# Optimization experiments

Hardware: AMD Instinct MI355X
Metric: run time of the kernel (lower is better)

## Reference

```python
import jax, jax.numpy as jnp
import numpy as np

N_NODES = 50000
N_EDGES = 800000


def gcn_layer(x, edge_index, W, b):
    """PyG-style GCNConv: add self-loops, symmetric deg^-1/2 normalization,
    linear transform, scatter-sum aggregation at target nodes, plus bias."""
    n = x.shape[0]
    loops = jnp.arange(n)
    src = jnp.concatenate([edge_index[0], loops])  # [E+N]
    dst = jnp.concatenate([edge_index[1], loops])  # [E+N]
    deg = jax.ops.segment_sum(jnp.ones(src.shape, dtype=x.dtype), dst, num_segments=n)
    dinv = jnp.where(deg > 0, jax.lax.rsqrt(deg), jnp.zeros((), x.dtype))
    norm = dinv[src] * dinv[dst]               # [E+N]
    h = x @ W                                   # [N, out]
    msg = norm[:, None] * h[src]                # [E+N, out] gather
    out = jax.ops.segment_sum(msg, dst, num_segments=n)  # scatter-add
    return out + b


def setup_inputs() -> dict:
    key = jax.random.key(0)
    ks = jax.random.split(key, 8)
    features = jax.random.normal(ks[0], (N_NODES, 64), dtype=jnp.float32)
    edge_index1 = jax.random.randint(ks[1], (2, N_EDGES), 0, N_NODES)
    edge_index3 = jax.random.randint(ks[2], (2, N_EDGES), 0, N_NODES)
    edge_index9 = jax.random.randint(ks[3], (2, N_EDGES), 0, N_NODES)

    def glorot(k, fi, fo):
        lim = float(np.sqrt(6.0 / (fi + fo)))
        return jax.random.uniform(k, (fi, fo), minval=-lim, maxval=lim, dtype=jnp.float32)

    W1 = glorot(ks[4], 64, 64)
    W2 = glorot(ks[5], 64, 32)
    W3 = glorot(ks[6], 32, 16)
    b1 = jnp.zeros((64,), jnp.float32)
    b2 = jnp.zeros((32,), jnp.float32)
    b3 = jnp.zeros((16,), jnp.float32)
    return dict(features=features, edge_index1=edge_index1, edge_index3=edge_index3,
                edge_index9=edge_index9, W1=W1, b1=b1, W2=W2, b2=b2, W3=W3, b3=b3)


def reference(features, edge_index1, edge_index3, edge_index9, W1, b1, W2, b2, W3, b3):
    x = jax.nn.relu(gcn_layer(features, edge_index1, W1, b1))  # hop 1
    x = jax.nn.relu(gcn_layer(x, edge_index3, W2, b2))         # hop 3
    x = jax.nn.relu(gcn_layer(x, edge_index9, W3, b3))         # hop 9
    return x
```

## Files before the change

kernel.cpp:

```cpp
#include <hip/hip_runtime.h>
#include <hip/hip_fp16.h>


#define NB   256
#define NL   3
#define TB   (NB * NL)
#define CAPE 6400
#define CAPE_E (CAPE + 8)
#define CH   8192
#define P1T  512
#define EPT  (CH / P1T)
#define P2T  512

__device__ __forceinline__ void decode_chunk(int g, int nc1, int nc2,
                                             const int* s1, const int* d1, int E1,
                                             const int* s2, const int* d2, int E2,
                                             const int* s3, const int* d3, int E3,
                                             const int** src, const int** dst, int* E, int* l,
                                             int* gout) {
    if (g < nc1)            { *src = s1; *dst = d1; *E = E1; *l = 0; }
    else if (g < nc1 + nc2) { *src = s2; *dst = d2; *E = E2; *l = 1; g -= nc1; }
    else                    { *src = s3; *dst = d3; *E = E3; *l = 2; g -= nc1 + nc2; }
    *gout = g;
}

__device__ __forceinline__ void fma4(float4& a, float s, const float4& w) {
    a.x += s * w.x; a.y += s * w.y; a.z += s * w.z; a.w += s * w.w;
}
__device__ __forceinline__ void add4(float4& a, const float4& v) {
    a.x += v.x; a.y += v.y; a.z += v.z; a.w += v.w;
}
__device__ __forceinline__ float4 ldh4(const __half* h, size_t idx4) {
    uint2 r = ((const uint2*)h)[idx4];
    __half2 a = *reinterpret_cast<__half2*>(&r.x);
    __half2 b = *reinterpret_cast<__half2*>(&r.y);
    float2 fa = __half22float2(a), fb = __half22float2(b);
    return make_float4(fa.x, fa.y, fb.x, fb.y);
}
__device__ __forceinline__ void sth4(__half* h, size_t idx4, float4 v) {
    __half2 a = __floats2half2_rn(v.x, v.y);
    __half2 b = __floats2half2_rn(v.z, v.w);
    uint2 r;
    r.x = *reinterpret_cast<unsigned*>(&a);
    r.y = *reinterpret_cast<unsigned*>(&b);
    ((uint2*)h)[idx4] = r;
}

__global__ void __launch_bounds__(P1T) phase1(
        const int* __restrict__ s1, const int* __restrict__ d1, int E1,
        const int* __restrict__ s2, const int* __restrict__ d2, int E2,
        const int* __restrict__ s3, const int* __restrict__ d3, int E3,
        int nc1, int nc2, int W,
        int* __restrict__ gcur, unsigned int* __restrict__ pairBuf) {
    __shared__ int hist[TB];
    __shared__ int bo[TB];
    __shared__ int lcur[TB];
    for (int i = threadIdx.x; i < TB; i += P1T) hist[i] = 0;
    __syncthreads();
    const int* src; const int* dst; int E, l, g;
    decode_chunk(blockIdx.x, nc1, nc2, s1, d1, E1, s2, d2, E2, s3, d3, E3,
                 &src, &dst, &E, &l, &g);
    const int e0 = g * CH;
    const int lbase = l * NB;
    unsigned pv[EPT];
    int bn[EPT];
    if (E - e0 >= CH) {
        const int4* s4 = (const int4*)(src + e0);
        const int4* d4 = (const int4*)(dst + e0);
#pragma unroll
        for (int w = 0; w < EPT / 4; ++w) {
            int4 sv = s4[threadIdx.x + w * P1T];
            int4 dv = d4[threadIdx.x + w * P1T];
            int q, i = w * 4;
            q = dv.x / W; bn[i+0] = lbase + q; pv[i+0] = ((unsigned)sv.x << 9) | (unsigned)(dv.x - q * W);
            q = dv.y / W; bn[i+1] = lbase + q; pv[i+1] = ((unsigned)sv.y << 9) | (unsigned)(dv.y - q * W);
            q = dv.z / W; bn[i+2] = lbase + q; pv[i+2] = ((unsigned)sv.z << 9) | (unsigned)(dv.z - q * W);
            q = dv.w / W; bn[i+3] = lbase + q; pv[i+3] = ((unsigned)sv.w << 9) | (unsigned)(dv.w - q * W);
        }
    } else {
#pragma unroll
        for (int i = 0; i < EPT; ++i) {
            int e = e0 + threadIdx.x + i * P1T;
            if (e < E) {
                int s = src[e], d = dst[e];
                int q = d / W;
                bn[i] = lbase + q;
                pv[i] = ((unsigned)s << 9) | (unsigned)(d - q * W);
            } else bn[i] = -1;
        }
    }
#pragma unroll
    for (int i = 0; i < EPT; ++i)
        if (bn[i] >= 0) atomicAdd(&hist[bn[i]], 1);
    __syncthreads();
    for (int i = threadIdx.x; i < TB; i += P1T) {
        int c = hist[i];
        bo[i] = i * CAPE + (c ? atomicAdd(&gcur[i], c) : 0);
        lcur[i] = 0;
    }
    __syncthreads();
#pragma unroll
    for (int i = 0; i < EPT; ++i) {
        if (bn[i] >= 0) {
            int r = atomicAdd(&lcur[bn[i]], 1);
            int pos = bo[bn[i]] + r;
            if (pos < (bn[i] + 1) * CAPE) pairBuf[pos] = pv[i];
        }
    }
}

__global__ void __launch_bounds__(P2T) k2_phase2_gemm1(
        const unsigned int* __restrict__ pairBuf, const int* __restrict__ gcur,
        int n, int W,
        int* __restrict__ row_ptr, int* __restrict__ cnt_g,
        float* __restrict__ dinv, unsigned short* __restrict__ eidx,
        const float* __restrict__ x0, const float* __restrict__ W1g,
        __half* __restrict__ h1) {
    __shared__ __align__(16) char smem[17408];
    if (blockIdx.x < (unsigned)TB) {
        int* lcnt  = (int*)smem;
        int* lscan = lcnt + P2T;
        unsigned short* stage = (unsigned short*)(lscan + P2T);
        const int bid = blockIdx.x;
        const int l = bid / NB, k = bid % NB;
        const int lo = k * W;
        const int hi = min(n, lo + W);
        const int Wn = hi - lo;
        const int segE = min(gcur[bid], CAPE);
        const size_t base  = (size_t)bid * CAPE;
        const int    baseE = bid * CAPE_E;
        const int t = threadIdx.x;
        lcnt[t] = 0;
        __syncthreads();
        for (int i = t; i < segE; i += P2T)
            atomicAdd(&lcnt[pairBuf[base + i] & 511u], 1);
        __syncthreads();
        const int v = lcnt[t];
        const int vp = (v + 3) & ~3;
        lscan[t] = vp;
        __syncthreads();
        for (int off = 1; off < P2T; off <<= 1) {
            int add = (t >= off) ? lscan[t - off] : 0;
            __syncthreads();
            lscan[t] += add;
            __syncthreads();
        }
        const int pexcl = lscan[t] - vp;
        const int segEp = lscan[P2T - 1];
        if (t < Wn) {
            int node = l * n + lo + t;
            row_ptr[node] = baseE + pexcl;
            cnt_g[node] = v;
            dinv[node] = rsqrtf((float)v + 1.0f);
        }
        __syncthreads();
        lcnt[t] = pexcl;
        __syncthreads();
        const bool lds_ok = (segEp <= CAPE);
        for (int i = t; i < segE; i += P2T) {
            unsigned p = pairBuf[base + i];
            int pos = atomicAdd(&lcnt[p & 511u], 1);
            unsigned short s = (unsigned short)(p >> 9);
            if (lds_ok) stage[pos] = s;
            else if (pos < CAPE_E) eidx[baseE + pos] = s;
        }
        __syncthreads();
        if (lds_ok) {
            const int4* st4 = (const int4*)stage;
            int4* e4 = (int4*)(eidx + baseE);
            int m16 = (segEp + 7) >> 3;
            for (int i = t; i < m16; i += P2T) e4[i] = st4[i];
        }
    } else {
        float* Ws = (float*)smem;
        const int bid = blockIdx.x - TB;
        for (int i = threadIdx.x; i < 1024; i += P2T)
            ((float4*)Ws)[i] = ((const float4*)W1g)[i];
        __syncthreads();
        const int tc = threadIdx.x % 16;
        const int tr = threadIdx.x / 16;
        const int row0 = bid * 128 + tr * 4;
        const float4* x4 = (const float4*)x0;
        const float4* Ws4 = (const float4*)Ws;
        float4 acc[4];
#pragma unroll
        for (int r = 0; r < 4; ++r) acc[r] = make_float4(0.f, 0.f, 0.f, 0.f);
        int rowc[4];
#pragma unroll
        for (int r = 0; r < 4; ++r) rowc[r] = min(row0 + r, n - 1);
        for (int k0 = 0; k0 < 64; k0 += 4) {
            float4 wv0 = Ws4[(k0 + 0) * 16 + tc];
            float4 wv1 = Ws4[(k0 + 1) * 16 + tc];
            float4 wv2 = Ws4[(k0 + 2) * 16 + tc];
            float4 wv3 = Ws4[(k0 + 3) * 16 + tc];
#pragma unroll
            for (int r = 0; r < 4; ++r) {
                float4 xv = x4[(size_t)rowc[r] * 16 + (k0 / 4)];
                fma4(acc[r], xv.x, wv0);
                fma4(acc[r], xv.y, wv1);
                fma4(acc[r], xv.z, wv2);
                fma4(acc[r], xv.w, wv3);
            }
        }
#pragma unroll
        for (int r = 0; r < 4; ++r) {
            int row = row0 + r;
            if (row < n) sth4(h1, (size_t)row * 16 + tc, acc[r]);
        }
    }
}

__global__ void __launch_bounds__(256) k3_gather1_gemm2(
        const int* __restrict__ row_ptr, const int* __restrict__ cnt,
        const unsigned short* __restrict__ eidx, const float* __restrict__ dinv1,
        const float* __restrict__ dinv2,
        const __half* __restrict__ h1, const float* __restrict__ b1,
        const float* __restrict__ W2g, __half* __restrict__ h2, int n) {
    __shared__ float xs[16 * 68];
    __shared__ float W2s[64 * 32];
    for (int i = threadIdx.x; i < 512; i += 256)
        ((float4*)W2s)[i] = ((const float4*)W2g)[i];
    const int ln = threadIdx.x >> 4;
    const int f4 = threadIdx.x & 15;
    const int node = blockIdx.x * 16 + ln;
    if (node < n) {
        const int beg = row_ptr[node];
        const int m = cnt[node];
        float4 a0 = make_float4(0.f, 0.f, 0.f, 0.f), a1 = a0, a2 = a0, a3 = a0;
        int j = 0;
        for (; j + 8 <= m; j += 8) {
            ushort4 e0 = *(const ushort4*)(eidx + beg + j);
            ushort4 e1 = *(const ushort4*)(eidx + beg + j + 4);
            float w0 = dinv1[e0.x], w1 = dinv1[e0.y], w2 = dinv1[e0.z], w3 = dinv1[e0.w];
            float w4 = dinv1[e1.x], w5 = dinv1[e1.y], w6 = dinv1[e1.z], w7 = dinv1[e1.w];
            float4 v0 = ldh4(h1, (size_t)e0.x * 16 + f4);
            float4 v1 = ldh4(h1, (size_t)e0.y * 16 + f4);
            float4 v2 = ldh4(h1, (size_t)e0.z * 16 + f4);
            float4 v3 = ldh4(h1, (size_t)e0.w * 16 + f4);
            float4 v4 = ldh4(h1, (size_t)e1.x * 16 + f4);
            float4 v5 = ldh4(h1, (size_t)e1.y * 16 + f4);
            float4 v6 = ldh4(h1, (size_t)e1.z * 16 + f4);
            float4 v7 = ldh4(h1, (size_t)e1.w * 16 + f4);
            fma4(a0, w0, v0); fma4(a1, w1, v1); fma4(a2, w2, v2); fma4(a3, w3, v3);
            fma4(a0, w4, v4); fma4(a1, w5, v5); fma4(a2, w6, v6); fma4(a3, w7, v7);
        }
        if (j + 4 <= m) {
            ushort4 e0 = *(const ushort4*)(eidx + beg + j);
            fma4(a0, dinv1[e0.x], ldh4(h1, (size_t)e0.x * 16 + f4));
            fma4(a1, dinv1[e0.y], ldh4(h1, (size_t)e0.y * 16 + f4));
            fma4(a2, dinv1[e0.z], ldh4(h1, (size_t)e0.z * 16 + f4));
            fma4(a3, dinv1[e0.w], ldh4(h1, (size_t)e0.w * 16 + f4));
            j += 4;
        }
        for (; j < m; ++j) {
            int s = eidx[beg + j];
            fma4(a0, dinv1[s], ldh4(h1, (size_t)s * 16 + f4));
        }
        add4(a0, a1); add4(a2, a3); add4(a0, a2);
        float di = dinv1[node];
        float4 self = ldh4(h1, (size_t)node * 16 + f4);
        float4 bv = ((const float4*)b1)[f4];
        float4 o;
        o.x = di * (a0.x + di * self.x) + bv.x;
        o.y = di * (a0.y + di * self.y) + bv.y;
        o.z = di * (a0.z + di * self.z) + bv.z;
        o.w = di * (a0.w + di * self.w) + bv.w;
        o.x = o.x > 0.f ? o.x : 0.f;
        o.y = o.y > 0.f ? o.y : 0.f;
        o.z = o.z > 0.f ? o.z : 0.f;
        o.w = o.w > 0.f ? o.w : 0.f;
        *(float4*)&xs[ln * 68 + f4 * 4] = o;
    }
    __syncthreads();
    if (node < n) {
        const int c0 = f4 * 2;
        float s0 = 0.f, s1 = 0.f;
#pragma unroll
        for (int k = 0; k < 64; ++k) {
            float xv = xs[ln * 68 + k];
            s0 += xv * W2s[k * 32 + c0];
            s1 += xv * W2s[k * 32 + c0 + 1];
        }
        float d2 = dinv2[node];
        ((__half2*)h2)[(size_t)node * 16 + f4] = __floats2half2_rn(s0 * d2, s1 * d2);
    }
}

__global__ void __launch_bounds__(256) k4_gather2_gemm3(
        const int* __restrict__ row_ptr2, const int* __restrict__ cnt2,
        const unsigned short* __restrict__ eidx, const float* __restrict__ dinv2,
        const float* __restrict__ dinv3,
        const __half* __restrict__ h2, const float* __restrict__ b2,
        const float* __restrict__ W3g, __half* __restrict__ h3, int n) {
    __shared__ float xs[32 * 36];
    __shared__ float W3s[32 * 16];
    for (int i = threadIdx.x; i < 128; i += 256)
        ((float4*)W3s)[i] = ((const float4*)W3g)[i];
    const int ln = threadIdx.x >> 3;
    const int f4 = threadIdx.x & 7;
    const int node = blockIdx.x * 32 + ln;
    if (node < n) {
        const int beg = row_ptr2[node];
        const int m = cnt2[node];
        float4 a0 = make_float4(0.f, 0.f, 0.f, 0.f), a1 = a0, a2 = a0, a3 = a0;
        int j = 0;
        for (; j + 8 <= m; j += 8) {
            ushort4 e0 = *(const ushort4*)(eidx + beg + j);
            ushort4 e1 = *(const ushort4*)(eidx + beg + j + 4);
            add4(a0, ldh4(h2, (size_t)e0.x * 8 + f4));
            add4(a1, ldh4(h2, (size_t)e0.y * 8 + f4));
            add4(a2, ldh4(h2, (size_t)e0.z * 8 + f4));
            add4(a3, ldh4(h2, (size_t)e0.w * 8 + f4));
            add4(a0, ldh4(h2, (size_t)e1.x * 8 + f4));
            add4(a1, ldh4(h2, (size_t)e1.y * 8 + f4));
            add4(a2, ldh4(h2, (size_t)e1.z * 8 + f4));
            add4(a3, ldh4(h2, (size_t)e1.w * 8 + f4));
        }
        if (j + 4 <= m) {
            ushort4 e0 = *(const ushort4*)(eidx + beg + j);
            add4(a0, ldh4(h2, (size_t)e0.x * 8 + f4));
            add4(a1, ldh4(h2, (size_t)e0.y * 8 + f4));
            add4(a2, ldh4(h2, (size_t)e0.z * 8 + f4));
            add4(a3, ldh4(h2, (size_t)e0.w * 8 + f4));
            j += 4;
        }
        for (; j < m; ++j)
            add4(a0, ldh4(h2, (size_t)eidx[beg + j] * 8 + f4));
        add4(a0, a1); add4(a2, a3); add4(a0, a2);
        float di = dinv2[node];
        float4 self = ldh4(h2, (size_t)node * 8 + f4);
        float4 bv = ((const float4*)b2)[f4];
        float4 o;
        o.x = di * (a0.x + self.x) + bv.x;
        o.y = di * (a0.y + self.y) + bv.y;
        o.z = di * (a0.z + self.z) + bv.z;
        o.w = di * (a0.w + self.w) + bv.w;
        o.x = o.x > 0.f ? o.x : 0.f;
        o.y = o.y > 0.f ? o.y : 0.f;
        o.z = o.z > 0.f ? o.z : 0.f;
        o.w = o.w > 0.f ? o.w : 0.f;
        *(float4*)&xs[ln * 36 + f4 * 4] = o;
    }
    __syncthreads();
    if (node < n) {
        const int c0 = f4 * 2;
        float s0 = 0.f, s1 = 0.f;
#pragma unroll
        for (int k = 0; k < 32; ++k) {
            float xv = xs[ln * 36 + k];
            s0 += xv * W3s[k * 16 + c0];
            s1 += xv * W3s[k * 16 + c0 + 1];
        }
        float d3 = dinv3[node];
        ((__half2*)h3)[(size_t)node * 8 + f4] = __floats2half2_rn(s0 * d3, s1 * d3);
    }
}

__global__ void __launch_bounds__(256) k5_gather3(
        const int* __restrict__ row_ptr3, const int* __restrict__ cnt3,
        const unsigned short* __restrict__ eidx, const float* __restrict__ dinv3,
        const __half* __restrict__ h3, const float* __restrict__ b3,
        float* __restrict__ out, int n) {
    const int ln = threadIdx.x >> 2;
    const int f4 = threadIdx.x & 3;
    const int node = blockIdx.x * 64 + ln;
    if (node >= n) return;
    const int beg = row_ptr3[node];
    const int m = cnt3[node];
    float4 a0 = make_float4(0.f, 0.f, 0.f, 0.f), a1 = a0, a2 = a0, a3 = a0;
    int j = 0;
    for (; j + 8 <= m; j += 8) {
        ushort4 e0 = *(const ushort4*)(eidx + beg + j);
        ushort4 e1 = *(const ushort4*)(eidx + beg + j + 4);
        add4(a0, ldh4(h3, (size_t)e0.x * 4 + f4));
        add4(a1, ldh4(h3, (size_t)e0.y * 4 + f4));
        add4(a2, ldh4(h3, (size_t)e0.z * 4 + f4));
        add4(a3, ldh4(h3, (size_t)e0.w * 4 + f4));
        add4(a0, ldh4(h3, (size_t)e1.x * 4 + f4));
        add4(a1, ldh4(h3, (size_t)e1.y * 4 + f4));
        add4(a2, ldh4(h3, (size_t)e1.z * 4 + f4));
        add4(a3, ldh4(h3, (size_t)e1.w * 4 + f4));
    }
    if (j + 4 <= m) {
        ushort4 e0 = *(const ushort4*)(eidx + beg + j);
        add4(a0, ldh4(h3, (size_t)e0.x * 4 + f4));
        add4(a1, ldh4(h3, (size_t)e0.y * 4 + f4));
        add4(a2, ldh4(h3, (size_t)e0.z * 4 + f4));
        add4(a3, ldh4(h3, (size_t)e0.w * 4 + f4));
        j += 4;
    }
    for (; j < m; ++j)
        add4(a0, ldh4(h3, (size_t)eidx[beg + j] * 4 + f4));
    add4(a0, a1); add4(a2, a3); add4(a0, a2);
    float di = dinv3[node];
    float4 self = ldh4(h3, (size_t)node * 4 + f4);
    float4 bv = ((const float4*)b3)[f4];
    float4 o;
    o.x = di * (a0.x + self.x) + bv.x;
    o.y = di * (a0.y + self.y) + bv.y;
    o.z = di * (a0.z + self.z) + bv.z;
    o.w = di * (a0.w + self.w) + bv.w;
    o.x = o.x > 0.f ? o.x : 0.f;
    o.y = o.y > 0.f ? o.y : 0.f;
    o.z = o.z > 0.f ? o.z : 0.f;
    o.w = o.w > 0.f ? o.w : 0.f;
    ((float4*)out)[(size_t)node * 4 + f4] = o;
}

extern "C" void kernel_launch(void* const* d_in, const int* in_sizes, int n_in,
                              void* d_out, int out_size, void* d_ws, size_t ws_size,
                              hipStream_t stream) {
    const float* x0  = (const float*)d_in[0];
    const int*   ei1 = (const int*)d_in[1];
    const int*   ei3 = (const int*)d_in[2];
    const int*   ei9 = (const int*)d_in[3];
    const float* W1  = (const float*)d_in[4];
    const float* b1  = (const float*)d_in[5];
    const float* W2  = (const float*)d_in[6];
    const float* b2  = (const float*)d_in[7];
    const float* W3  = (const float*)d_in[8];
    const float* b3  = (const float*)d_in[9];

    const int n  = in_sizes[0] / 64;
    const int E1 = in_sizes[1] / 2;
    const int E3 = in_sizes[2] / 2;
    const int E9 = in_sizes[3] / 2;
    const int n3 = 3 * n;
    const int W  = (n + NB - 1) / NB;

    const int nc1 = (E1 + CH - 1) / CH;
    const int nc2 = (E3 + CH - 1) / CH;
    const int nc3 = (E9 + CH - 1) / CH;
    const int nchunks = nc1 + nc2 + nc3;
    const int gemmBlks = (n + 127) / 128;

    int* gcur    = (int*)d_ws;
    unsigned int* pairBuf = (unsigned int*)(gcur + TB);
    unsigned short* eidx = (unsigned short*)(pairBuf + (size_t)TB * CAPE);
    int* row_ptr = (int*)(eidx + (size_t)TB * CAPE_E);
    int* cnt     = row_ptr + n3;
    float* dinv  = (float*)(cnt + n3);
    __half* h1   = (__half*)(dinv + n3);
    __half* h2   = h1 + (size_t)n * 64;
    __half* h3   = h2 + (size_t)n * 32;

    hipMemsetAsync(gcur, 0, TB * sizeof(int), stream);
    phase1<<<nchunks, P1T, 0, stream>>>(ei1, ei1 + E1, E1, ei3, ei3 + E3, E3,
                                        ei9, ei9 + E9, E9, nc1, nc2, W, gcur, pairBuf);
    k2_phase2_gemm1<<<TB + gemmBlks, P2T, 0, stream>>>(
        pairBuf, gcur, n, W, row_ptr, cnt, dinv, eidx, x0, W1, h1);
    k3_gather1_gemm2<<<(n + 15) / 16, 256, 0, stream>>>(
        row_ptr, cnt, eidx, dinv, dinv + n, h1, b1, W2, h2, n);
    k4_gather2_gemm3<<<(n + 31) / 32, 256, 0, stream>>>(
        row_ptr + n, cnt + n, eidx, dinv + n, dinv + 2 * n, h2, b2, W3, h3, n);
    k5_gather3<<<(n + 63) / 64, 256, 0, stream>>>(
        row_ptr + 2 * n, cnt + 2 * n, eidx, dinv + 2 * n, h3, b3, (float*)d_out, n);
}
```

Measured before the change: 176.8 us.

## Sort nodes by degree within buckets to balance gather workloads

The phase-2 kernel now counting-sorts each bucket's nodes by descending in-degree and writes a per-layer node permutation. The three gather kernels process nodes in permuted order, so nodes of similar degree share a block and wavefront. This aims to cut divergence and tail imbalance inside warps, at the cost of an extra sort, an extra indirection load, and scattered output writes. The node ids are stored as unsigned short, so the permutation only holds while n fits in 16 bits.

```diff
diff --git a/kernel.cpp b/kernel.cpp
--- a/kernel.cpp
+++ b/kernel.cpp
@@ -114,6 +114,7 @@
         int n, int W,
         int* __restrict__ row_ptr, int* __restrict__ cnt_g,
         float* __restrict__ dinv, unsigned short* __restrict__ eidx,
+        unsigned short* __restrict__ nodeperm,
         const float* __restrict__ x0, const float* __restrict__ W1g,
         __half* __restrict__ h1) {
     __shared__ __align__(16) char smem[17408];
@@ -171,6 +172,31 @@
             int m16 = (segEp + 7) >> 3;
             for (int i = t; i < m16; i += P2T) e4[i] = st4[i];
         }
+        __syncthreads();
+        int* dcnt = lcnt;
+        int* dscan = lscan;
+        if (t < 256) dcnt[t] = 0;
+        __syncthreads();
+        int r = 0;
+        if (t < Wn) {
+            r = 255 - min(v, 255);
+            atomicAdd(&dcnt[r], 1);
+        }
+        __syncthreads();
+        if (t < 256) dscan[t] = dcnt[t];
+        __syncthreads();
+        for (int off = 1; off < 256; off <<= 1) {
+            int add = (t < 256 && t >= off) ? dscan[t - off] : 0;
+            __syncthreads();
+            if (t < 256) dscan[t] += add;
+            __syncthreads();
+        }
+        if (t < 256) dcnt[t] = dscan[t] - dcnt[t];
+        __syncthreads();
+        if (t < Wn) {
+            int slot = atomicAdd(&dcnt[r], 1);
+            nodeperm[(size_t)l * n + lo + slot] = (unsigned short)(lo + t);
+        }
     } else {
         float* Ws = (float*)smem;
         const int bid = blockIdx.x - TB;
@@ -184,28 +210,28 @@
         const float4* Ws4 = (const float4*)Ws;
         float4 acc[4];
 #pragma unroll
-        for (int r = 0; r < 4; ++r) acc[r] = make_float4(0.f, 0.f, 0.f, 0.f);
+        for (int r2 = 0; r2 < 4; ++r2) acc[r2] = make_float4(0.f, 0.f, 0.f, 0.f);
         int rowc[4];
 #pragma unroll
-        for (int r = 0; r < 4; ++r) rowc[r] = min(row0 + r, n - 1);
+        for (int r2 = 0; r2 < 4; ++r2) rowc[r2] = min(row0 + r2, n - 1);
         for (int k0 = 0; k0 < 64; k0 += 4) {
             float4 wv0 = Ws4[(k0 + 0) * 16 + tc];
             float4 wv1 = Ws4[(k0 + 1) * 16 + tc];
             float4 wv2 = Ws4[(k0 + 2) * 16 + tc];
             float4 wv3 = Ws4[(k0 + 3) * 16 + tc];
 #pragma unroll
-            for (int r = 0; r < 4; ++r) {
-                float4 xv = x4[(size_t)rowc[r] * 16 + (k0 / 4)];
-                fma4(acc[r], xv.x, wv0);
-                fma4(acc[r], xv.y, wv1);
-                fma4(acc[r], xv.z, wv2);
-                fma4(acc[r], xv.w, wv3);
+            for (int r2 = 0; r2 < 4; ++r2) {
+                float4 xv = x4[(size_t)rowc[r2] * 16 + (k0 / 4)];
+                fma4(acc[r2], xv.x, wv0);
+                fma4(acc[r2], xv.y, wv1);
+                fma4(acc[r2], xv.z, wv2);
+                fma4(acc[r2], xv.w, wv3);
             }
         }
 #pragma unroll
-        for (int r = 0; r < 4; ++r) {
-            int row = row0 + r;
-            if (row < n) sth4(h1, (size_t)row * 16 + tc, acc[r]);
+        for (int r2 = 0; r2 < 4; ++r2) {
+            int row = row0 + r2;
+            if (row < n) sth4(h1, (size_t)row * 16 + tc, acc[r2]);
         }
     }
 }
@@ -213,7 +239,7 @@
 __global__ void __launch_bounds__(256) k3_gather1_gemm2(
         const int* __restrict__ row_ptr, const int* __restrict__ cnt,
         const unsigned short* __restrict__ eidx, const float* __restrict__ dinv1,
-        const float* __restrict__ dinv2,
+        const float* __restrict__ dinv2, const unsigned short* __restrict__ perm,
         const __half* __restrict__ h1, const float* __restrict__ b1,
         const float* __restrict__ W2g, __half* __restrict__ h2, int n) {
     __shared__ float xs[16 * 68];
@@ -222,8 +248,9 @@
         ((float4*)W2s)[i] = ((const float4*)W2g)[i];
     const int ln = threadIdx.x >> 4;
     const int f4 = threadIdx.x & 15;
-    const int node = blockIdx.x * 16 + ln;
-    if (node < n) {
+    const int g = blockIdx.x * 16 + ln;
+    const int node = (g < n) ? (int)perm[g] : -1;
+    if (node >= 0) {
         const int beg = row_ptr[node];
         const int m = cnt[node];
         float4 a0 = make_float4(0.f, 0.f, 0.f, 0.f), a1 = a0, a2 = a0, a3 = a0;
@@ -272,7 +299,7 @@
         *(float4*)&xs[ln * 68 + f4 * 4] = o;
     }
     __syncthreads();
-    if (node < n) {
+    if (node >= 0) {
         const int c0 = f4 * 2;
         float s0 = 0.f, s1 = 0.f;
 #pragma unroll
@@ -289,7 +316,7 @@
 __global__ void __launch_bounds__(256) k4_gather2_gemm3(
         const int* __restrict__ row_ptr2, const int* __restrict__ cnt2,
         const unsigned short* __restrict__ eidx, const float* __restrict__ dinv2,
-        const float* __restrict__ dinv3,
+        const float* __restrict__ dinv3, const unsigned short* __restrict__ perm,
         const __half* __restrict__ h2, const float* __restrict__ b2,
         const float* __restrict__ W3g, __half* __restrict__ h3, int n) {
     __shared__ float xs[32 * 36];
@@ -298,8 +325,9 @@
         ((float4*)W3s)[i] = ((const float4*)W3g)[i];
     const int ln = threadIdx.x >> 3;
     const int f4 = threadIdx.x & 7;
-    const int node = blockIdx.x * 32 + ln;
-    if (node < n) {
+    const int g = blockIdx.x * 32 + ln;
+    const int node = (g < n) ? (int)perm[g] : -1;
+    if (node >= 0) {
         const int beg = row_ptr2[node];
         const int m = cnt2[node];
         float4 a0 = make_float4(0.f, 0.f, 0.f, 0.f), a1 = a0, a2 = a0, a3 = a0;
@@ -342,7 +370,7 @@
         *(float4*)&xs[ln * 36 + f4 * 4] = o;
     }
     __syncthreads();
-    if (node < n) {
+    if (node >= 0) {
         const int c0 = f4 * 2;
         float s0 = 0.f, s1 = 0.f;
 #pragma unroll
@@ -359,12 +387,14 @@
 __global__ void __launch_bounds__(256) k5_gather3(
         const int* __restrict__ row_ptr3, const int* __restrict__ cnt3,
         const unsigned short* __restrict__ eidx, const float* __restrict__ dinv3,
+        const unsigned short* __restrict__ perm,
         const __half* __restrict__ h3, const float* __restrict__ b3,
         float* __restrict__ out, int n) {
     const int ln = threadIdx.x >> 2;
     const int f4 = threadIdx.x & 3;
-    const int node = blockIdx.x * 64 + ln;
-    if (node >= n) return;
+    const int g = blockIdx.x * 64 + ln;
+    if (g >= n) return;
+    const int node = (int)perm[g];
     const int beg = row_ptr3[node];
     const int m = cnt3[node];
     float4 a0 = make_float4(0.f, 0.f, 0.f, 0.f), a1 = a0, a2 = a0, a3 = a0;
@@ -437,7 +467,8 @@
     int* gcur    = (int*)d_ws;
     unsigned int* pairBuf = (unsigned int*)(gcur + TB);
     unsigned short* eidx = (unsigned short*)(pairBuf + (size_t)TB * CAPE);
-    int* row_ptr = (int*)(eidx + (size_t)TB * CAPE_E);
+    unsigned short* nodeperm = eidx + (size_t)TB * CAPE_E;
+    int* row_ptr = (int*)(nodeperm + ((size_t)n3 + 8));
     int* cnt     = row_ptr + n3;
     float* dinv  = (float*)(cnt + n3);
     __half* h1   = (__half*)(dinv + n3);
@@ -448,11 +479,12 @@
     phase1<<<nchunks, P1T, 0, stream>>>(ei1, ei1 + E1, E1, ei3, ei3 + E3, E3,
                                         ei9, ei9 + E9, E9, nc1, nc2, W, gcur, pairBuf);
     k2_phase2_gemm1<<<TB + gemmBlks, P2T, 0, stream>>>(
-        pairBuf, gcur, n, W, row_ptr, cnt, dinv, eidx, x0, W1, h1);
+        pairBuf, gcur, n, W, row_ptr, cnt, dinv, eidx, nodeperm, x0, W1, h1);
     k3_gather1_gemm2<<<(n + 15) / 16, 256, 0, stream>>>(
-        row_ptr, cnt, eidx, dinv, dinv + n, h1, b1, W2, h2, n);
+        row_ptr, cnt, eidx, dinv, dinv + n, nodeperm, h1, b1, W2, h2, n);
     k4_gather2_gemm3<<<(n + 31) / 32, 256, 0, stream>>>(
-        row_ptr + n, cnt + n, eidx, dinv + n, dinv + 2 * n, h2, b2, W3, h3, n);
+        row_ptr + n, cnt + n, eidx, dinv + n, dinv + 2 * n, nodeperm + n, h2, b2, W3, h3, n);
     k5_gather3<<<(n + 63) / 64, 256, 0, stream>>>(
-        row_ptr + 2 * n, cnt + 2 * n, eidx, dinv + 2 * n, h3, b3, (float*)d_out, n);
-}
+        row_ptr + 2 * n, cnt + 2 * n, eidx, dinv + 2 * n, nodeperm + 2 * n, h3, b3,
+        (float*)d_out, n);
+}
```

Result: slower. 183.7 us (+3.9%).
